# Performance work log

Measured on AMD Instinct MI355X. Metric: run time of the kernel, lower is better.

## Reference

```python
import jax, jax.numpy as jnp
import numpy as np


def setup_inputs() -> dict:
    key = jax.random.key(0)
    ks = jax.random.split(key, 7)
    B, S, D_IN, D_K, D_V = 4, 4096, 1024, 64, 64
    s = 1.0 / np.sqrt(D_IN)
    return {
        "query": jax.random.normal(ks[0], (B, S, D_IN), jnp.float32),
        "key": jax.random.normal(ks[1], (B, S, D_IN), jnp.float32),
        "value": jax.random.normal(ks[2], (B, S, D_IN), jnp.float32),
        "Wq": jax.random.normal(ks[3], (D_IN, D_K), jnp.float32) * s,
        "bq": jnp.zeros((D_K,), jnp.float32),
        "Wk": jax.random.normal(ks[4], (D_IN, D_K), jnp.float32) * s,
        "bk": jnp.zeros((D_K,), jnp.float32),
        "Wv": jax.random.normal(ks[5], (D_IN, D_V), jnp.float32) * s,
        "bv": jnp.zeros((D_V,), jnp.float32),
    }


def reference(query, key, value, Wq, bq, Wk, bk, Wv, bv):
    # q(query) is computed twice in the original but is identical; compute once.
    q = query @ Wq + bq            # [B,S,dk]
    k = key @ Wk + bk              # [B,S,dk]
    v = value @ Wv + bv            # [B,S,dv]
    scale = jnp.asarray(q.shape[-1] ** 0.5, q.dtype)
    scores = jnp.einsum("bqd,bkd->bqk", q, k) / scale  # [B,S,S]
    probs = jax.nn.softmax(scores, axis=-1)
    return jnp.einsum("bqk,bkd->bqd", probs, v)        # [B,S,dv]
```

## Files before the change

### kernel.cpp

```cpp
#include <hip/hip_runtime.h>
#include <cmath>

constexpr int B_  = 4;
constexpr int S_  = 4096;
constexpr int DIN = 1024;
constexpr int DH  = 64;

typedef short bf16x8 __attribute__((ext_vector_type(8)));
typedef float f32x4  __attribute__((ext_vector_type(4)));

#define GPTR(p) (const __attribute__((address_space(1))) unsigned int*)(p)
#define LPTR(p) (__attribute__((address_space(3))) unsigned int*)(p)

__device__ __forceinline__ ushort f2bf(float x) {
    unsigned int u = __float_as_uint(x);
    return (ushort)((u + 0x7FFFu + ((u >> 16) & 1u)) >> 16);
}

__device__ __forceinline__ bf16x8 cvt8(float4 a, float4 b) {
    union { bf16x8 v; ushort u[8]; } r;
    r.u[0] = f2bf(a.x); r.u[1] = f2bf(a.y); r.u[2] = f2bf(a.z); r.u[3] = f2bf(a.w);
    r.u[4] = f2bf(b.x); r.u[5] = f2bf(b.y); r.u[6] = f2bf(b.z); r.u[7] = f2bf(b.w);
    return r.v;
}

#define QSCALE 0.18033688011112042f

__global__ __launch_bounds__(256) void setup_w(
    const float* __restrict__ Wq, const float* __restrict__ Wk,
    const float* __restrict__ Wv, ushort* __restrict__ Wt_g)
{
    const int y = blockIdx.y;
    const float* W = (y == 0) ? Wq : (y == 1) ? Wk : Wv;
    const int g    = blockIdx.x * 256 + threadIdx.x;
    const int lane = g & 63;
    const int nt   = (g >> 6) & 3;
    const int ks   = (g >> 8) & 1;
    const int it   = g >> 9;
    const int m    = lane & 15;
    const int quad = lane >> 4;
    const int n    = nt * 16 + m;
    const int k0   = it * 64 + (ks * 4 + quad) * 8;
    union { uint4 q; ushort u[8]; } r;
    #pragma unroll
    for (int i = 0; i < 8; ++i) r.u[i] = f2bf(W[(size_t)(k0 + i) * DH + n]);
    *(uint4*)(Wt_g + ((size_t)y << 16) + (size_t)g * 8) = r.q;
}

__global__ __launch_bounds__(256, 3) void proj_kernel(
    const float* __restrict__ Xq, const float* __restrict__ Xk, const float* __restrict__ Xv,
    const float* __restrict__ bq, const float* __restrict__ bk, const float* __restrict__ bv,
    const ushort* __restrict__ Wt_g,
    ushort* __restrict__ Qb, ushort* __restrict__ Kb, ushort* __restrict__ Vt)
{
    const int y = blockIdx.y;
    const float *X, *bias;
    if (y == 0)      { X = Xq; bias = bq; }
    else if (y == 1) { X = Xk; bias = bk; }
    else             { X = Xv; bias = bv; }

    __shared__ ushort Vx[64 * 72];

    const int tid  = threadIdx.x;
    const int w    = tid >> 6;
    const int lane = tid & 63;
    const int m    = lane & 15;
    const int quad = lane >> 4;
    const int row0 = blockIdx.x * 64;

    const size_t  xrow = (size_t)(row0 + w * 16 + m) * DIN;
    const ushort* wsrc = Wt_g + ((size_t)y << 16) + (size_t)lane * 8;

    float bias_v[4];
    #pragma unroll
    for (int nt = 0; nt < 4; ++nt) bias_v[nt] = bias[nt * 16 + m];

    f32x4 acc[4] = {};
    float4 xb[2][4];
    uint4  wb[2][8];

    {
        const float* px = X + xrow + quad * 8;
        xb[0][0] = *(const float4*)(px);      xb[0][1] = *(const float4*)(px + 4);
        xb[0][2] = *(const float4*)(px + 32); xb[0][3] = *(const float4*)(px + 36);
        #pragma unroll
        for (int f = 0; f < 8; ++f)
            wb[0][f] = *(const uint4*)(wsrc + (size_t)f * 512);
    }

    #pragma unroll
    for (int it = 0; it < 16; ++it) {
        const int cb = it & 1, nb = cb ^ 1;
        if (it < 15) {
            const float* px = X + xrow + (it + 1) * 64 + quad * 8;
            xb[nb][0] = *(const float4*)(px);      xb[nb][1] = *(const float4*)(px + 4);
            xb[nb][2] = *(const float4*)(px + 32); xb[nb][3] = *(const float4*)(px + 36);
            #pragma unroll
            for (int f = 0; f < 8; ++f)
                wb[nb][f] = *(const uint4*)(wsrc + (size_t)((it + 1) * 8 + f) * 512);
        }
        #pragma unroll
        for (int ks = 0; ks < 2; ++ks) {
            const bf16x8 a = cvt8(xb[cb][ks * 2], xb[cb][ks * 2 + 1]);
            #pragma unroll
            for (int nt = 0; nt < 4; ++nt)
                acc[nt] = __builtin_amdgcn_mfma_f32_16x16x32_bf16(
                    a, *(const bf16x8*)&wb[cb][ks * 4 + nt], acc[nt], 0, 0, 0);
        }
    }

    if (y < 2) {
        ushort* Out = (y == 0) ? Qb : Kb;
        const float sc = (y == 0) ? QSCALE : 1.0f;
        #pragma unroll
        for (int nt = 0; nt < 4; ++nt)
            #pragma unroll
            for (int j = 0; j < 4; ++j) {
                const int row = row0 + w * 16 + quad * 4 + j;
                Out[(size_t)row * DH + nt * 16 + m] = f2bf((acc[nt][j] + bias_v[nt]) * sc);
            }
    } else {
        #pragma unroll
        for (int nt = 0; nt < 4; ++nt)
            #pragma unroll
            for (int j = 0; j < 4; ++j) {
                const int d = nt * 16 + m;
                const int s = w * 16 + quad * 4 + j;
                Vx[d * 72 + (((s >> 3) ^ (d & 7)) * 8) + (s & 7)] = f2bf(acc[nt][j] + bias_v[nt]);
            }
        __syncthreads();
        const int batch = row0 >> 12;
        const int s0    = row0 & 4095;
        for (int i = tid; i < 512; i += 256) {
            const int d = i >> 3, c = i & 7;
            const uint4 v = *(const uint4*)&Vx[d * 72 + ((c ^ (d & 7)) * 8)];
            *(uint4*)(Vt + ((size_t)batch * 64 + d) * S_ + s0 + c * 8) = v;
        }
    }
}

__global__ __launch_bounds__(256, 4) void attn_kernel(
    const ushort* __restrict__ Qb, const ushort* __restrict__ Kb,
    const ushort* __restrict__ Vt, float* __restrict__ Opart, float* __restrict__ Lpart)
{
    __shared__ ushort Ks[64 * 64];
    __shared__ ushort Vs[64 * 64];
    __shared__ ushort Pt[64 * 72];

    const int tid  = threadIdx.x;
    const int w    = tid >> 6;
    const int lane = tid & 63;
    const int m    = lane & 15;
    const int quad = lane >> 4;
    const int b    = blockIdx.z, jc = blockIdx.y, qt = blockIdx.x;
    const int q0   = qt * 64;

    bf16x8 qf[2];
    #pragma unroll
    for (int ks = 0; ks < 2; ++ks)
        qf[ks] = *(const bf16x8*)(Qb + (size_t)(b * S_ + q0 + w * 16 + m) * 64
                                     + ks * 32 + quad * 8);

    f32x4 acc_o[4] = {};
    float Lp[4] = {};

    const ushort* kbase = Kb + (size_t)b * S_ * 64;
    const ushort* vbase = Vt + (size_t)b * 64 * S_;

    for (int it = 0; it < 16; ++it) {
        const int jt = jc * 16 + it;
        __syncthreads();
        #pragma unroll
        for (int i = 0; i < 2; ++i) {
            const int slot = w * 128 + i * 64 + lane;
            const int j = slot >> 3, c = slot & 7;
            __builtin_amdgcn_global_load_lds(
                GPTR(kbase + (size_t)(jt * 64 + j) * 64 + ((c ^ (j & 7)) * 8)),
                LPTR(&Ks[(w * 128 + i * 64) * 8]), 16, 0, 0);
            __builtin_amdgcn_global_load_lds(
                GPTR(vbase + (size_t)j * S_ + jt * 64 + ((c ^ (j & 7)) * 8)),
                LPTR(&Vs[(w * 128 + i * 64) * 8]), 16, 0, 0);
        }
        __syncthreads();

        f32x4 acc_s[4] = {};
        #pragma unroll
        for (int ks = 0; ks < 2; ++ks)
            #pragma unroll
            for (int jt4 = 0; jt4 < 4; ++jt4) {
                const int j = jt4 * 16 + m;
                const bf16x8 kf = *(const bf16x8*)&Ks[j * 64 + (((ks * 4 + quad) ^ (j & 7)) * 8)];
                acc_s[jt4] = __builtin_amdgcn_mfma_f32_16x16x32_bf16(
                    qf[ks], kf, acc_s[jt4], 0, 0, 0);
            }

        #pragma unroll
        for (int jt4 = 0; jt4 < 4; ++jt4)
            #pragma unroll
            for (int r = 0; r < 4; ++r) {
                const float e = exp2f(acc_s[jt4][r]);
                Lp[r] += e;
                Pt[(w * 16 + quad * 4 + r) * 72 + jt4 * 16 + m] = f2bf(e);
            }

        #pragma unroll
        for (int jc2 = 0; jc2 < 2; ++jc2) {
            const bf16x8 pf = *(const bf16x8*)&Pt[(w * 16 + m) * 72 + jc2 * 32 + quad * 8];
            #pragma unroll
            for (int dt = 0; dt < 4; ++dt) {
                const int d = dt * 16 + m;
                const bf16x8 vf = *(const bf16x8*)&Vs[d * 64 + (((jc2 * 4 + quad) ^ (d & 7)) * 8)];
                acc_o[dt] = __builtin_amdgcn_mfma_f32_16x16x32_bf16(pf, vf, acc_o[dt], 0, 0, 0);
            }
        }
    }

    #pragma unroll
    for (int r = 0; r < 4; ++r) {
        float s = Lp[r];
        #pragma unroll
        for (int off = 1; off < 16; off <<= 1)
            s += __shfl_xor(s, off, 64);
        Lp[r] = s;
    }

    const size_t bj = (size_t)(b * 4 + jc);
    float* Ob = Opart + (bj << 18);
    #pragma unroll
    for (int dt = 0; dt < 4; ++dt)
        #pragma unroll
        for (int r = 0; r < 4; ++r) {
            const int row = q0 + w * 16 + quad * 4 + r;
            Ob[(size_t)row * 64 + dt * 16 + m] = acc_o[dt][r];
        }
    if (m == 0) {
        #pragma unroll
        for (int r = 0; r < 4; ++r)
            Lpart[bj * 4096 + q0 + w * 16 + quad * 4 + r] = Lp[r];
    }
}

__global__ __launch_bounds__(256) void reduce_kernel(
    const float* __restrict__ Opart, const float* __restrict__ Lpart, float* __restrict__ out)
{
    const int g    = blockIdx.x * 256 + threadIdx.x;
    const int base = g << 2;
    const int b    = base >> 18;
    const int rem  = base & 0x3FFFF;
    const int q    = rem >> 6;
    float4 o = make_float4(0.f, 0.f, 0.f, 0.f);
    float  l = 0.f;
    #pragma unroll
    for (int jcc = 0; jcc < 4; ++jcc) {
        const float4 p = *(const float4*)(Opart + (((size_t)(b * 4 + jcc)) << 18) + rem);
        o.x += p.x; o.y += p.y; o.z += p.z; o.w += p.w;
        l += Lpart[(size_t)(b * 4 + jcc) * 4096 + q];
    }
    const float inv = 1.0f / l;
    o.x *= inv; o.y *= inv; o.z *= inv; o.w *= inv;
    *(float4*)(out + base) = o;
}

extern "C" void kernel_launch(void* const* d_in, const int* in_sizes, int n_in,
                              void* d_out, int out_size, void* d_ws, size_t ws_size,
                              hipStream_t stream)
{
    const float* query = (const float*)d_in[0];
    const float* key_  = (const float*)d_in[1];
    const float* value = (const float*)d_in[2];
    const float* Wq    = (const float*)d_in[3];
    const float* bq    = (const float*)d_in[4];
    const float* Wk    = (const float*)d_in[5];
    const float* bk    = (const float*)d_in[6];
    const float* Wv    = (const float*)d_in[7];
    const float* bv    = (const float*)d_in[8];
    float* out = (float*)d_out;

    char* ws = (char*)d_ws;
    ushort* Qb    = (ushort*)(ws);
    ushort* Kb    = (ushort*)(ws + (2  << 20));
    ushort* Vt    = (ushort*)(ws + (4  << 20));
    float*  Opart = (float*) (ws + (6  << 20));
    float*  Lpart = (float*) (ws + (22 << 20));
    ushort* Wt_g  = (ushort*)(ws + (6  << 20));

    setup_w<<<dim3(32, 3), 256, 0, stream>>>(Wq, Wk, Wv, Wt_g);
    proj_kernel<<<dim3(256, 3), 256, 0, stream>>>(
        query, key_, value, bq, bk, bv, Wt_g, Qb, Kb, Vt);
    attn_kernel<<<dim3(64, 4, 4), 256, 0, stream>>>(Qb, Kb, Vt, Opart, Lpart);
    reduce_kernel<<<dim3(1024), 256, 0, stream>>>(Opart, Lpart, out);
}
```

Before: 271.0 us.

## Deepen projection pipeline to four stages with async LDS weight loads

The projection kernel now keeps four k-steps in flight. X rows are loaded through inline-asm global_load_dwordx4 into register sets, and the bf16 weight tiles are copied straight into LDS with global_load_lds, all synchronised by explicit vmcnt waits and barriers. This replaces the register double-buffer that held the full weight fragments per thread. The goal is to hide HBM latency on this memory-bound stage and cut register pressure. In exchange it adds 32KB of shared memory, which can limit occupancy, two barriers per step, and fragile hand-counted vmcnt values.

Result: faster. 259.4 us (-4.3%).

```diff
diff --git a/kernel.cpp b/kernel.cpp
--- a/kernel.cpp
+++ b/kernel.cpp
@@ -11,16 +11,17 @@
 
 #define GPTR(p) (const __attribute__((address_space(1))) unsigned int*)(p)
 #define LPTR(p) (__attribute__((address_space(3))) unsigned int*)(p)
+#define LDSB8(p) (*(const __attribute__((address_space(3))) bf16x8*)(p))
 
 __device__ __forceinline__ ushort f2bf(float x) {
     unsigned int u = __float_as_uint(x);
     return (ushort)((u + 0x7FFFu + ((u >> 16) & 1u)) >> 16);
 }
 
-__device__ __forceinline__ bf16x8 cvt8(float4 a, float4 b) {
+__device__ __forceinline__ bf16x8 cvt8(f32x4 a, f32x4 b) {
     union { bf16x8 v; ushort u[8]; } r;
-    r.u[0] = f2bf(a.x); r.u[1] = f2bf(a.y); r.u[2] = f2bf(a.z); r.u[3] = f2bf(a.w);
-    r.u[4] = f2bf(b.x); r.u[5] = f2bf(b.y); r.u[6] = f2bf(b.z); r.u[7] = f2bf(b.w);
+    r.u[0] = f2bf(a[0]); r.u[1] = f2bf(a[1]); r.u[2] = f2bf(a[2]); r.u[3] = f2bf(a[3]);
+    r.u[4] = f2bf(b[0]); r.u[5] = f2bf(b[1]); r.u[6] = f2bf(b[2]); r.u[7] = f2bf(b[3]);
     return r.v;
 }
 
@@ -47,19 +48,57 @@
     *(uint4*)(Wt_g + ((size_t)y << 16) + (size_t)g * 8) = r.q;
 }
 
+#define WAITV(NLIT) asm volatile("s_waitcnt vmcnt(" NLIT ")" ::: "memory")
+#define XLOAD(dst, OFFLIT) \
+    asm volatile("global_load_dwordx4 %0, %1, off offset:" OFFLIT \
+                 : "=v"(dst) : "v"(xa) : "memory")
+#define ISSUE_X(S) do { \
+    XLOAD(xs##S##_0, "0");   XLOAD(xs##S##_1, "16"); \
+    XLOAD(xs##S##_2, "128"); XLOAD(xs##S##_3, "144"); } while (0)
+#define ISSUE_W(WI, S) do { \
+    char* wdst_ = smem + (S) * 8192; \
+    __builtin_amdgcn_global_load_lds(GPTR(wsrc + (size_t)((WI)*8 + w*2    )*1024 + lane*16), \
+                                     LPTR(wdst_ + (w*2    )*1024 + lane*16), 16, 0, 0); \
+    __builtin_amdgcn_global_load_lds(GPTR(wsrc + (size_t)((WI)*8 + w*2 + 1)*1024 + lane*16), \
+                                     LPTR(wdst_ + (w*2 + 1)*1024 + lane*16), 16, 0, 0); } while (0)
+#define COMPUTE(S) do { \
+    const char* wb_ = smem + (S) * 8192; \
+    const bf16x8 a0 = cvt8(xs##S##_0, xs##S##_1); \
+    const bf16x8 a1 = cvt8(xs##S##_2, xs##S##_3); \
+    _Pragma("unroll") \
+    for (int nt = 0; nt < 4; ++nt) \
+        acc[nt] = __builtin_amdgcn_mfma_f32_16x16x32_bf16(a0, LDSB8(wb_ + nt*1024 + lane*16), acc[nt], 0, 0, 0); \
+    _Pragma("unroll") \
+    for (int nt = 0; nt < 4; ++nt) \
+        acc[nt] = __builtin_amdgcn_mfma_f32_16x16x32_bf16(a1, LDSB8(wb_ + (4+nt)*1024 + lane*16), acc[nt], 0, 0, 0); } while (0)
+#define STEP(IT, S, VMLIT) do { \
+    WAITV(VMLIT); \
+    __builtin_amdgcn_sched_barrier(0); \
+    __builtin_amdgcn_s_barrier(); \
+    __builtin_amdgcn_sched_barrier(0); \
+    COMPUTE(S); \
+    __builtin_amdgcn_sched_barrier(0); \
+    __builtin_amdgcn_s_barrier(); \
+    __builtin_amdgcn_sched_barrier(0); \
+    if ((IT) + 4 < 16) { \
+        const uint64_t xa = xbase + (uint64_t)((IT) + 4) * 256; \
+        ISSUE_X(S); \
+        ISSUE_W((IT) + 4, S); \
+    } } while (0)
+
 __global__ __launch_bounds__(256, 3) void proj_kernel(
     const float* __restrict__ Xq, const float* __restrict__ Xk, const float* __restrict__ Xv,
     const float* __restrict__ bq, const float* __restrict__ bk, const float* __restrict__ bv,
     const ushort* __restrict__ Wt_g,
     ushort* __restrict__ Qb, ushort* __restrict__ Kb, ushort* __restrict__ Vt)
 {
+    __shared__ __align__(16) char smem[32768];
+
     const int y = blockIdx.y;
     const float *X, *bias;
     if (y == 0)      { X = Xq; bias = bq; }
     else if (y == 1) { X = Xk; bias = bk; }
     else             { X = Xv; bias = bv; }
-
-    __shared__ ushort Vx[64 * 72];
 
     const int tid  = threadIdx.x;
     const int w    = tid >> 6;
@@ -68,46 +107,30 @@
     const int quad = lane >> 4;
     const int row0 = blockIdx.x * 64;
 
-    const size_t  xrow = (size_t)(row0 + w * 16 + m) * DIN;
-    const ushort* wsrc = Wt_g + ((size_t)y << 16) + (size_t)lane * 8;
-
     float bias_v[4];
     #pragma unroll
     for (int nt = 0; nt < 4; ++nt) bias_v[nt] = bias[nt * 16 + m];
-
+    asm volatile("s_waitcnt vmcnt(0)" ::: "memory");
+    __builtin_amdgcn_sched_barrier(0);
+
+    const char*    wsrc  = (const char*)Wt_g + ((size_t)y << 17);
+    const uint64_t xbase = (uint64_t)(uintptr_t)(X + (size_t)(row0 + w * 16 + m) * DIN + quad * 8);
+
+    f32x4 xs0_0, xs0_1, xs0_2, xs0_3;
+    f32x4 xs1_0, xs1_1, xs1_2, xs1_3;
+    f32x4 xs2_0, xs2_1, xs2_2, xs2_3;
+    f32x4 xs3_0, xs3_1, xs3_2, xs3_3;
     f32x4 acc[4] = {};
-    float4 xb[2][4];
-    uint4  wb[2][8];
-
-    {
-        const float* px = X + xrow + quad * 8;
-        xb[0][0] = *(const float4*)(px);      xb[0][1] = *(const float4*)(px + 4);
-        xb[0][2] = *(const float4*)(px + 32); xb[0][3] = *(const float4*)(px + 36);
-        #pragma unroll
-        for (int f = 0; f < 8; ++f)
-            wb[0][f] = *(const uint4*)(wsrc + (size_t)f * 512);
-    }
-
-    #pragma unroll
-    for (int it = 0; it < 16; ++it) {
-        const int cb = it & 1, nb = cb ^ 1;
-        if (it < 15) {
-            const float* px = X + xrow + (it + 1) * 64 + quad * 8;
-            xb[nb][0] = *(const float4*)(px);      xb[nb][1] = *(const float4*)(px + 4);
-            xb[nb][2] = *(const float4*)(px + 32); xb[nb][3] = *(const float4*)(px + 36);
-            #pragma unroll
-            for (int f = 0; f < 8; ++f)
-                wb[nb][f] = *(const uint4*)(wsrc + (size_t)((it + 1) * 8 + f) * 512);
-        }
-        #pragma unroll
-        for (int ks = 0; ks < 2; ++ks) {
-            const bf16x8 a = cvt8(xb[cb][ks * 2], xb[cb][ks * 2 + 1]);
-            #pragma unroll
-            for (int nt = 0; nt < 4; ++nt)
-                acc[nt] = __builtin_amdgcn_mfma_f32_16x16x32_bf16(
-                    a, *(const bf16x8*)&wb[cb][ks * 4 + nt], acc[nt], 0, 0, 0);
-        }
-    }
+
+    { const uint64_t xa = xbase;                    ISSUE_X(0); ISSUE_W(0, 0); }
+    { const uint64_t xa = xbase + 256;              ISSUE_X(1); ISSUE_W(1, 1); }
+    { const uint64_t xa = xbase + 512;              ISSUE_X(2); ISSUE_W(2, 2); }
+    { const uint64_t xa = xbase + 768;              ISSUE_X(3); ISSUE_W(3, 3); }
+
+    STEP( 0, 0, "18"); STEP( 1, 1, "18"); STEP( 2, 2, "18"); STEP( 3, 3, "18");
+    STEP( 4, 0, "18"); STEP( 5, 1, "18"); STEP( 6, 2, "18"); STEP( 7, 3, "18");
+    STEP( 8, 0, "18"); STEP( 9, 1, "18"); STEP(10, 2, "18"); STEP(11, 3, "18");
+    STEP(12, 0, "18"); STEP(13, 1, "12"); STEP(14, 2, "6");  STEP(15, 3, "0");
 
     if (y < 2) {
         ushort* Out = (y == 0) ? Qb : Kb;
@@ -116,10 +139,12 @@
         for (int nt = 0; nt < 4; ++nt)
             #pragma unroll
             for (int j = 0; j < 4; ++j) {
-                const int row = row0 + w * 16 + quad * 4 + j;
-                Out[(size_t)row * DH + nt * 16 + m] = f2bf((acc[nt][j] + bias_v[nt]) * sc);
+                const int r = row0 + w * 16 + quad * 4 + j;
+                Out[(size_t)r * DH + nt * 16 + m] = f2bf((acc[nt][j] + bias_v[nt]) * sc);
             }
     } else {
+        __syncthreads();
+        ushort* Vx = (ushort*)smem;
         #pragma unroll
         for (int nt = 0; nt < 4; ++nt)
             #pragma unroll
```

## Restructure projection to stage coalesced bf16 X rows in LDS, smaller tiles

Applied to the files above, without the earlier changes.

The projection kernel now handles 16 rows per block instead of 64, launching four times as many blocks. Each block loads its X rows with fully coalesced float4 reads, converts them to bf16 once, and stores them in XOR-swizzled LDS. Each wave then computes one 16-column output tile, reading A fragments from LDS and streaming weight fragments with double buffering. The goal is better DRAM coalescing and more parallelism on a memory-bound stage. The cost is that every block re-reads the full bf16 weight matrix, so total weight traffic through L2 rises by about four times.

Result: faster. 252.0 us (-7.0%).

```diff
diff --git a/kernel.cpp b/kernel.cpp
--- a/kernel.cpp
+++ b/kernel.cpp
@@ -17,10 +17,10 @@
     return (ushort)((u + 0x7FFFu + ((u >> 16) & 1u)) >> 16);
 }
 
-__device__ __forceinline__ bf16x8 cvt8(float4 a, float4 b) {
+__device__ __forceinline__ bf16x8 cvt8(f32x4 a, f32x4 b) {
     union { bf16x8 v; ushort u[8]; } r;
-    r.u[0] = f2bf(a.x); r.u[1] = f2bf(a.y); r.u[2] = f2bf(a.z); r.u[3] = f2bf(a.w);
-    r.u[4] = f2bf(b.x); r.u[5] = f2bf(b.y); r.u[6] = f2bf(b.z); r.u[7] = f2bf(b.w);
+    r.u[0] = f2bf(a[0]); r.u[1] = f2bf(a[1]); r.u[2] = f2bf(a[2]); r.u[3] = f2bf(a[3]);
+    r.u[4] = f2bf(b[0]); r.u[5] = f2bf(b[1]); r.u[6] = f2bf(b[2]); r.u[7] = f2bf(b[3]);
     return r.v;
 }
 
@@ -47,94 +47,94 @@
     *(uint4*)(Wt_g + ((size_t)y << 16) + (size_t)g * 8) = r.q;
 }
 
-__global__ __launch_bounds__(256, 3) void proj_kernel(
+__global__ __launch_bounds__(256, 4) void proj_kernel(
     const float* __restrict__ Xq, const float* __restrict__ Xk, const float* __restrict__ Xv,
     const float* __restrict__ bq, const float* __restrict__ bk, const float* __restrict__ bv,
     const ushort* __restrict__ Wt_g,
     ushort* __restrict__ Qb, ushort* __restrict__ Kb, ushort* __restrict__ Vt)
 {
+    __shared__ __align__(16) ushort xlds[16384];
+
     const int y = blockIdx.y;
     const float *X, *bias;
     if (y == 0)      { X = Xq; bias = bq; }
     else if (y == 1) { X = Xk; bias = bk; }
     else             { X = Xv; bias = bv; }
 
-    __shared__ ushort Vx[64 * 72];
-
     const int tid  = threadIdx.x;
     const int w    = tid >> 6;
     const int lane = tid & 63;
     const int m    = lane & 15;
     const int quad = lane >> 4;
-    const int row0 = blockIdx.x * 64;
-
-    const size_t  xrow = (size_t)(row0 + w * 16 + m) * DIN;
-    const ushort* wsrc = Wt_g + ((size_t)y << 16) + (size_t)lane * 8;
-
-    float bias_v[4];
-    #pragma unroll
-    for (int nt = 0; nt < 4; ++nt) bias_v[nt] = bias[nt * 16 + m];
-
-    f32x4 acc[4] = {};
-    float4 xb[2][4];
-    uint4  wb[2][8];
+    const int row0 = blockIdx.x * 16;
 
     {
-        const float* px = X + xrow + quad * 8;
-        xb[0][0] = *(const float4*)(px);      xb[0][1] = *(const float4*)(px + 4);
-        xb[0][2] = *(const float4*)(px + 32); xb[0][3] = *(const float4*)(px + 36);
-        #pragma unroll
-        for (int f = 0; f < 8; ++f)
-            wb[0][f] = *(const uint4*)(wsrc + (size_t)f * 512);
-    }
-
-    #pragma unroll
-    for (int it = 0; it < 16; ++it) {
-        const int cb = it & 1, nb = cb ^ 1;
-        if (it < 15) {
-            const float* px = X + xrow + (it + 1) * 64 + quad * 8;
-            xb[nb][0] = *(const float4*)(px);      xb[nb][1] = *(const float4*)(px + 4);
-            xb[nb][2] = *(const float4*)(px + 32); xb[nb][3] = *(const float4*)(px + 36);
-            #pragma unroll
-            for (int f = 0; f < 8; ++f)
-                wb[nb][f] = *(const uint4*)(wsrc + (size_t)((it + 1) * 8 + f) * 512);
-        }
-        #pragma unroll
-        for (int ks = 0; ks < 2; ++ks) {
-            const bf16x8 a = cvt8(xb[cb][ks * 2], xb[cb][ks * 2 + 1]);
-            #pragma unroll
-            for (int nt = 0; nt < 4; ++nt)
-                acc[nt] = __builtin_amdgcn_mfma_f32_16x16x32_bf16(
-                    a, *(const bf16x8*)&wb[cb][ks * 4 + nt], acc[nt], 0, 0, 0);
-        }
+        f32x4 va[8], vb[8];
+        #pragma unroll
+        for (int r = 0; r < 4; ++r) {
+            const float* src = X + (size_t)(row0 + w * 4 + r) * DIN + lane * 8;
+            #pragma unroll
+            for (int sg = 0; sg < 2; ++sg) {
+                va[r * 2 + sg] = *(const f32x4*)(src + sg * 512);
+                vb[r * 2 + sg] = *(const f32x4*)(src + sg * 512 + 4);
+            }
+        }
+        __builtin_amdgcn_sched_barrier(0);
+        #pragma unroll
+        for (int r = 0; r < 4; ++r) {
+            const int row = w * 4 + r;
+            #pragma unroll
+            for (int sg = 0; sg < 2; ++sg) {
+                const int wi = sg * 8 + (lane >> 3);
+                const int fx = (lane & 7) ^ (row & 7);
+                *(bf16x8*)&xlds[((wi * 16 + row) * 8 + fx) * 8] =
+                    cvt8(va[r * 2 + sg], vb[r * 2 + sg]);
+            }
+        }
+    }
+    __syncthreads();
+
+    const float bias_v = bias[w * 16 + m];
+    const ushort* wbase = Wt_g + ((size_t)y << 16) + (size_t)(w * 64 + lane) * 8;
+
+    f32x4 acc = {};
+    bf16x8 wf0 = *(const bf16x8*)(wbase);
+    bf16x8 wf1 = *(const bf16x8*)(wbase + 2048);
+    #pragma unroll
+    for (int wi = 0; wi < 16; ++wi) {
+        bf16x8 nf0 = wf0, nf1 = wf1;
+        if (wi < 15) {
+            nf0 = *(const bf16x8*)(wbase + (size_t)(wi + 1) * 4096);
+            nf1 = *(const bf16x8*)(wbase + (size_t)(wi + 1) * 4096 + 2048);
+        }
+        const bf16x8 a0 = *(const bf16x8*)&xlds[((wi * 16 + m) * 8 + ( quad      ^ (m & 7))) * 8];
+        const bf16x8 a1 = *(const bf16x8*)&xlds[((wi * 16 + m) * 8 + ((4 + quad) ^ (m & 7))) * 8];
+        acc = __builtin_amdgcn_mfma_f32_16x16x32_bf16(a0, wf0, acc, 0, 0, 0);
+        acc = __builtin_amdgcn_mfma_f32_16x16x32_bf16(a1, wf1, acc, 0, 0, 0);
+        wf0 = nf0; wf1 = nf1;
     }
 
     if (y < 2) {
         ushort* Out = (y == 0) ? Qb : Kb;
         const float sc = (y == 0) ? QSCALE : 1.0f;
         #pragma unroll
-        for (int nt = 0; nt < 4; ++nt)
-            #pragma unroll
-            for (int j = 0; j < 4; ++j) {
-                const int row = row0 + w * 16 + quad * 4 + j;
-                Out[(size_t)row * DH + nt * 16 + m] = f2bf((acc[nt][j] + bias_v[nt]) * sc);
-            }
+        for (int j = 0; j < 4; ++j) {
+            const int row = row0 + quad * 4 + j;
+            Out[(size_t)row * DH + w * 16 + m] = f2bf((acc[j] + bias_v) * sc);
+        }
     } else {
-        #pragma unroll
-        for (int nt = 0; nt < 4; ++nt)
-            #pragma unroll
-            for (int j = 0; j < 4; ++j) {
-                const int d = nt * 16 + m;
-                const int s = w * 16 + quad * 4 + j;
-                Vx[d * 72 + (((s >> 3) ^ (d & 7)) * 8) + (s & 7)] = f2bf(acc[nt][j] + bias_v[nt]);
-            }
+        __syncthreads();
+        ushort (*Vx)[32] = (ushort(*)[32])xlds;
+        #pragma unroll
+        for (int j = 0; j < 4; ++j)
+            Vx[w * 16 + m][quad * 4 + j] = f2bf(acc[j] + bias_v);
         __syncthreads();
         const int batch = row0 >> 12;
         const int s0    = row0 & 4095;
-        for (int i = tid; i < 512; i += 256) {
-            const int d = i >> 3, c = i & 7;
-            const uint4 v = *(const uint4*)&Vx[d * 72 + ((c ^ (d & 7)) * 8)];
-            *(uint4*)(Vt + ((size_t)batch * 64 + d) * S_ + s0 + c * 8) = v;
+        if (tid < 128) {
+            const int d = tid >> 1, h = tid & 1;
+            const uint4 v = *(const uint4*)&Vx[d][h * 8];
+            *(uint4*)(Vt + ((size_t)batch * 64 + d) * S_ + s0 + h * 8) = v;
         }
     }
 }
@@ -285,7 +285,7 @@
     ushort* Wt_g  = (ushort*)(ws + (6  << 20));
 
     setup_w<<<dim3(32, 3), 256, 0, stream>>>(Wq, Wk, Wv, Wt_g);
-    proj_kernel<<<dim3(256, 3), 256, 0, stream>>>(
+    proj_kernel<<<dim3(1024, 3), 256, 0, stream>>>(
         query, key_, value, bq, bk, bv, Wt_g, Qb, Kb, Vt);
     attn_kernel<<<dim3(64, 4, 4), 256, 0, stream>>>(Qb, Kb, Vt, Opart, Lpart);
     reduce_kernel<<<dim3(1024), 256, 0, stream>>>(Opart, Lpart, out);
```
